# Kernel tuning notes

Hardware: AMD Instinct MI355X
Metric: run time of the kernel (lower is better)

The kernel has to match this reference:

```python
import jax, jax.numpy as jnp
import numpy as np

EPS = 1e-6

def _norm(x, alpha, beta):
    # torch std is unbiased (n-1); eps added to std (not var)
    d = x.shape[-1]
    mu = jnp.mean(x, axis=-1, keepdims=True)
    xc = x - mu
    std = jnp.sqrt(jnp.sum(xc * xc, axis=-1, keepdims=True) / (d - 1))
    return alpha * xc / (std + EPS) + beta

def setup_inputs() -> dict:
    key = jax.random.key(0)
    B, S, D, P, H, DFF = 4, 2048, 1024, 256, 16, 512
    ks = jax.random.split(key, 24)
    sd = 1.0 / np.sqrt(D)
    inp = {
        "feature_x": jax.random.normal(ks[0], (B, S, D), jnp.float32),
        "param_x": jax.random.normal(ks[1], (B, S, P), jnp.float32),
        "Wq": jax.random.normal(ks[2], (D, D), jnp.float32) * sd,
        "bq": jnp.zeros((D,), jnp.float32),
        "Wk": jax.random.normal(ks[3], (D, D), jnp.float32) * sd,
        "bk": jnp.zeros((D,), jnp.float32),
        "Wv": jax.random.normal(ks[4], (D, D), jnp.float32) * sd,
        "bv": jnp.zeros((D,), jnp.float32),
        "Wo": jax.random.normal(ks[5], (D, D), jnp.float32) * sd,
        "bo": jnp.zeros((D,), jnp.float32),
        "alpha1": jnp.ones((D,), jnp.float32),
        "beta1": jnp.zeros((D,), jnp.float32),
        "alpha2": jnp.ones((D,), jnp.float32),
        "beta2": jnp.zeros((D,), jnp.float32),
        "W1": jax.random.normal(ks[6], (D, DFF), jnp.float32) * sd,
        "b1": jnp.zeros((DFF,), jnp.float32),
        "W2": jax.random.normal(ks[7], (DFF, D), jnp.float32) / np.sqrt(DFF),
        "b2": jnp.zeros((D,), jnp.float32),
        "Wp": jax.random.normal(ks[8], (D + P, P), jnp.float32) / np.sqrt(D + P),
        "bp": jnp.zeros((P,), jnp.float32),
    }
    return inp

def reference(feature_x, param_x, Wq, bq, Wk, bk, Wv, bv, Wo, bo,
              alpha1, beta1, alpha2, beta2, W1, b1, W2, b2, Wp, bp):
    B, S, D = feature_x.shape
    H = 16
    dh = D // H
    # pre-norm (note: original reassigns feature_x = norm_1(feature_x))
    xn = _norm(feature_x, alpha1, beta1)
    q = (xn @ Wq + bq).reshape(B, S, H, dh)
    k = (xn @ Wk + bk).reshape(B, S, H, dh)
    v = (xn @ Wv + bv).reshape(B, S, H, dh)
    scores = jnp.einsum('bqhd,bkhd->bhqk', q, k) / jnp.sqrt(jnp.float32(dh))
    attn = jax.nn.softmax(scores, axis=-1)  # dropout = identity (eval)
    ctx = jnp.einsum('bhqk,bkhd->bqhd', attn, v).reshape(B, S, D)
    attn_out = ctx @ Wo + bo
    x = xn + attn_out
    x2 = _norm(x, alpha2, beta2)
    ff = jax.nn.relu(x2 @ W1 + b1) @ W2 + b2
    x = x + ff
    combined = jnp.concatenate([x, param_x], axis=-1)
    p = combined @ Wp + bp
    return (x, p)
```

## Files before the change

### kernel.cpp

```cpp
#include <hip/hip_runtime.h>
#include <hip/hip_bf16.h>

typedef unsigned short u16;
typedef short short8 __attribute__((ext_vector_type(8)));
typedef float f32x4 __attribute__((ext_vector_type(4)));

#define MELEM 8388608u
__device__ u16 g_ws[(size_t)MELEM * 13];

__device__ __forceinline__ float b2f(u16 u) {
  union { unsigned int i; float f; } v; v.i = ((unsigned int)u) << 16; return v.f;
}
__device__ __forceinline__ u16 f2b(float f) {
  union { float f; unsigned int i; } v; v.f = f;
  return (u16)((v.i + 0x7FFFu + ((v.i >> 16) & 1u)) >> 16);
}
__device__ __forceinline__ unsigned int pk2(float a, float b) {
  union { __hip_bfloat162 h; unsigned int u; } v;
  v.h = __float22bfloat162_rn(make_float2(a, b));
  return v.u;
}
__device__ __forceinline__ f32x4 mfma16(short8 a, short8 b, f32x4 c) {
  return __builtin_amdgcn_mfma_f32_16x16x32_bf16(a, b, c, 0, 0, 0);
}

typedef __attribute__((address_space(3))) unsigned int lds_u32;
typedef const __attribute__((address_space(1))) unsigned int glb_u32;
__device__ __forceinline__ void gld16(u16* l, const u16* g) {
  __builtin_amdgcn_global_load_lds((glb_u32*)g, (lds_u32*)l, 16, 0, 0);
}

#if __has_builtin(__builtin_amdgcn_exp2f)
#define QSCALE 0.18033688011112042f
#define SCLAMP 86.561714f
#define FEXP(x) __builtin_amdgcn_exp2f(x)
#else
#define QSCALE 0.125f
#define SCLAMP 60.0f
#define FEXP(x) __expf(x)
#endif

__device__ __forceinline__ void tr32(const float* __restrict__ W, u16* __restrict__ Wt,
                                     int K, int N, int bx, int by, int tid,
                                     float (*tile)[33]) {
  const int tx = tid & 31, ty = tid >> 5;
#pragma unroll
  for (int i = 0; i < 32; i += 8)
    tile[ty + i][tx] = W[(size_t)(by + ty + i) * N + bx + tx];
  __syncthreads();
#pragma unroll
  for (int i = 0; i < 32; i += 8)
    Wt[(size_t)(bx + ty + i) * K + by + tx] = f2b(tile[tx][ty + i]);
}

__global__ __launch_bounds__(256) void prep_kernel(
    const float* __restrict__ Wq, const float* __restrict__ Wk,
    const float* __restrict__ Wv, const float* __restrict__ Wo,
    const float* __restrict__ W1, const float* __restrict__ W2,
    const float* __restrict__ Wp,
    const float* __restrict__ bq, const float* __restrict__ bk,
    const float* __restrict__ bv, const float* __restrict__ param_x,
    u16* __restrict__ Wqkvt, u16* __restrict__ Wot, u16* __restrict__ W1t,
    u16* __restrict__ W2t, u16* __restrict__ Wpt,
    float* __restrict__ bqkv, u16* __restrict__ px_b) {
  __shared__ float tile[32][33];
  const int bid = blockIdx.x;
  const int tid = threadIdx.x;
  if (bid < 4096) {
    const int j = bid >> 10, r = bid & 1023;
    const int bx = (r & 31) * 32, by = (r >> 5) * 32;
    const float* src = (j == 0) ? Wq : (j == 1) ? Wk : (j == 2) ? Wv : Wo;
    u16* dst = (j == 3) ? Wot : (Wqkvt + (size_t)j * 1024 * 1024);
    tr32(src, dst, 1024, 1024, bx, by, tid, tile);
  } else if (bid < 4608) {
    const int r = bid - 4096;
    tr32(W1, W1t, 1024, 512, (r & 15) * 32, (r >> 4) * 32, tid, tile);
  } else if (bid < 5120) {
    const int r = bid - 4608;
    tr32(W2, W2t, 512, 1024, (r & 31) * 32, (r >> 5) * 32, tid, tile);
  } else if (bid < 5440) {
    const int r = bid - 5120;
    tr32(Wp, Wpt, 1280, 256, (r & 7) * 32, (r >> 3) * 32, tid, tile);
  } else if (bid < 5452) {
    const int i = (bid - 5440) * 256 + tid;
    bqkv[i] = (i < 1024) ? bq[i] : (i < 2048) ? bk[i - 1024] : bv[i - 2048];
  } else {
    const int i = (bid - 5452) * 256 + tid;
    px_b[i] = f2b(param_x[i]);
  }
}

__global__ __launch_bounds__(256) void ln_kernel(const float* __restrict__ x,
                                                 const float* __restrict__ alpha,
                                                 const float* __restrict__ beta,
                                                 u16* __restrict__ outb,
                                                 float* __restrict__ outf) {
  const int D = 1024;
  const int row = blockIdx.x;
  const int tid = threadIdx.x;
  const float4 u = *(const float4*)(x + (size_t)row * D + tid * 4);
  float s1 = u.x + u.y + u.z + u.w;
  float s2 = u.x * u.x + u.y * u.y + u.z * u.z + u.w * u.w;
#pragma unroll
  for (int off = 32; off >= 1; off >>= 1) {
    s1 += __shfl_xor(s1, off, 64);
    s2 += __shfl_xor(s2, off, 64);
  }
  __shared__ float ws1[4], ws2[4];
  if ((tid & 63) == 0) { ws1[tid >> 6] = s1; ws2[tid >> 6] = s2; }
  __syncthreads();
  s1 = ws1[0] + ws1[1] + ws1[2] + ws1[3];
  s2 = ws2[0] + ws2[1] + ws2[2] + ws2[3];
  const float mean = s1 * (1.0f / 1024.0f);
  const float var = fmaxf((s2 - 1024.0f * mean * mean) * (1.0f / 1023.0f), 0.0f);
  const float inv = 1.0f / (sqrtf(var) + 1e-6f);
  const float4 a = *(const float4*)(alpha + tid * 4);
  const float4 b = *(const float4*)(beta + tid * 4);
  const float o0 = a.x * (u.x - mean) * inv + b.x;
  const float o1 = a.y * (u.y - mean) * inv + b.y;
  const float o2 = a.z * (u.z - mean) * inv + b.z;
  const float o3 = a.w * (u.w - mean) * inv + b.w;
  ushort4 ob; ob.x = f2b(o0); ob.y = f2b(o1); ob.z = f2b(o2); ob.w = f2b(o3);
  *(ushort4*)(outb + (size_t)row * D + tid * 4) = ob;
  if (outf) {
    float4 of; of.x = o0; of.y = o1; of.z = o2; of.w = o3;
    *(float4*)(outf + (size_t)row * D + tid * 4) = of;
  }
}

template<int TM, int TN>
__global__ __launch_bounds__(256) void gemm_t(
    const u16* __restrict__ A, const u16* __restrict__ A2,
    const u16* __restrict__ Bt, const float* __restrict__ bias,
    const float* __restrict__ resid, float* __restrict__ Cf, u16* __restrict__ Cb,
    u16* __restrict__ Vt_out,
    int M, int N, int K, int K1, int relu, int ldcb) {
  __shared__ __align__(16) u16 As[TM * 32];
  __shared__ __align__(16) u16 Bs[TN * 32];
  const int tid = threadIdx.x;
  const int bn = blockIdx.x * TN;
  const int bm = blockIdx.y * TM;
  const int wv = tid >> 6, lane = tid & 63, quad = lane >> 4, l16 = lane & 15;
  constexpr int WN = (TM == 128) ? 64 : TN / 4;
  constexpr int AM = 4, AN = WN / 16;
  const int wm = (TM == 128) ? (wv >> 1) * 64 : 0;
  const int wn = (TM == 128) ? (wv & 1) * 64 : wv * WN;
  const int r0 = tid >> 2;
  const int cc = (tid & 3) * 8;
  f32x4 acc[AM][AN];
#pragma unroll
  for (int i = 0; i < AM; ++i)
#pragma unroll
    for (int j = 0; j < AN; ++j) acc[i][j] = (f32x4){0.f, 0.f, 0.f, 0.f};

  for (int k0 = 0; k0 < K; k0 += 32) {
    const u16* aS; int lda, kk;
    if (A2 != nullptr && k0 >= K1) { aS = A2; lda = K - K1; kk = k0 - K1; }
    else { aS = A; lda = (A2 != nullptr) ? K1 : K; kk = k0; }
#pragma unroll
    for (int i = 0; i < TM / 64; ++i)
      gld16(&As[i * 2048 + tid * 8], aS + (size_t)(bm + i * 64 + r0) * lda + kk + cc);
#pragma unroll
    for (int i = 0; i < TN / 64; ++i)
      gld16(&Bs[i * 2048 + tid * 8], Bt + (size_t)(bn + i * 64 + r0) * K + k0 + cc);
    __syncthreads();
    short8 af[AM], bf[AN];
#pragma unroll
    for (int mi = 0; mi < AM; ++mi)
      af[mi] = *(const short8*)&As[(wm + mi * 16 + l16) * 32 + quad * 8];
#pragma unroll
    for (int ni = 0; ni < AN; ++ni)
      bf[ni] = *(const short8*)&Bs[(wn + ni * 16 + l16) * 32 + quad * 8];
#pragma unroll
    for (int mi = 0; mi < AM; ++mi)
#pragma unroll
      for (int ni = 0; ni < AN; ++ni)
        acc[mi][ni] = mfma16(af[mi], bf[ni], acc[mi][ni]);
    __syncthreads();
  }

#pragma unroll
  for (int ni = 0; ni < AN; ++ni) {
    const int col = bn + wn + ni * 16 + l16;
    const float bb = bias ? bias[col] : 0.0f;
#pragma unroll
    for (int mi = 0; mi < AM; ++mi) {
      if (Vt_out != nullptr && col >= 2048) {
        const int s0 = bm + wm + mi * 16 + quad * 4;
        const int bb_idx = s0 >> 11;
        const size_t voff = ((size_t)(bb_idx * 1024 + col - 2048) << 11) + (s0 & 2047);
        ushort4 w;
        w.x = f2b(acc[mi][ni][0] + bb);
        w.y = f2b(acc[mi][ni][1] + bb);
        w.z = f2b(acc[mi][ni][2] + bb);
        w.w = f2b(acc[mi][ni][3] + bb);
        *(ushort4*)(Vt_out + voff) = w;
      } else {
#pragma unroll
        for (int r = 0; r < 4; ++r) {
          const int row = bm + wm + mi * 16 + quad * 4 + r;
          const size_t off = (size_t)row * N + col;
          float v = acc[mi][ni][r] + bb;
          if (resid) v += resid[off];
          if (relu) v = fmaxf(v, 0.0f);
          if (Cf) Cf[off] = v;
          if (Cb) Cb[(size_t)row * ldcb + col] = f2b(v);
        }
      }
    }
  }
}

__global__ __launch_bounds__(512) void attn_kernel(
    const u16* __restrict__ Q, const u16* __restrict__ Kb,
    const u16* __restrict__ Vtg, u16* __restrict__ O, int ldq) {
  const int S = 2048, NT = 32;
  __shared__ __align__(16) u16 Ks[2][64][64];
  __shared__ __align__(16) u16 Vs[2][64][64];
  __shared__ __align__(16) u16 Pb[8][32][40];
  const int tid = threadIdx.x;
  const int swz = ((blockIdx.x & 7) << 6) | (blockIdx.x >> 3);
  const int qt = swz & 7;
  const int bh = swz >> 3;
  const int b = bh >> 4, h = bh & 15;
  const int wv = tid >> 6, lane = tid & 63, quad = lane >> 4, l16 = lane & 15;
  const size_t brow = (size_t)b * S;
  const size_t hoff = (size_t)h * 64;
  const int q0 = qt * 256 + wv * 32;
  const u16* Vg = Vtg + (((size_t)(b * 1024 + h * 64)) << 11);

  short8 qf[2][2];
#pragma unroll
  for (int ni = 0; ni < 2; ++ni)
#pragma unroll
    for (int ks = 0; ks < 2; ++ks) {
      int4 t = *(const int4*)(Q + (brow + q0 + ni * 16 + l16) * ldq + hoff + ks * 32 + quad * 8);
      const u16* p = (const u16*)&t;
      short8 f;
#pragma unroll
      for (int j = 0; j < 8; ++j) f[j] = (short)f2b(b2f(p[j]) * QSCALE);
      qf[ni][ks] = f;
    }

  f32x4 oacc[4][2];
#pragma unroll
  for (int mi = 0; mi < 4; ++mi)
#pragma unroll
    for (int ni = 0; ni < 2; ++ni) oacc[mi][ni] = (f32x4){0.f, 0.f, 0.f, 0.f};
  float lsum[2] = {0.0f, 0.0f};
  const f32x4 z4 = {0.f, 0.f, 0.f, 0.f};

  const int srow = tid >> 3;
  const int sc = (tid & 7) ^ (srow & 7);

  gld16(&Ks[0][0][0] + (size_t)tid * 8, Kb + (brow + srow) * ldq + hoff + sc * 8);
  gld16(&Vs[0][0][0] + (size_t)tid * 8, Vg + ((size_t)srow << 11) + sc * 8);
  __syncthreads();

  for (int t = 0; t < NT; ++t) {
    const int p = t & 1, np = p ^ 1;
    if (t + 1 < NT) {
      const int kbn = (t + 1) * 64;
      gld16(&Ks[np][0][0] + (size_t)tid * 8, Kb + (brow + kbn + srow) * ldq + hoff + sc * 8);
      gld16(&Vs[np][0][0] + (size_t)tid * 8, Vg + ((size_t)srow << 11) + kbn + sc * 8);
    }

    const u16* ksb = &Ks[p][0][0];
    const u16* vsb = &Vs[p][0][0];
#pragma unroll
    for (int kk = 0; kk < 2; ++kk) {
#pragma unroll
      for (int half = 0; half < 2; ++half) {
        const int m = (kk * 2 + half) * 16 + l16;
        short8 af0 = *(const short8*)(ksb + m * 64 + ((quad ^ (m & 7)) * 8));
        short8 af1 = *(const short8*)(ksb + m * 64 + (((4 + quad) ^ (m & 7)) * 8));
#pragma unroll
        for (int ni = 0; ni < 2; ++ni) {
          f32x4 s = z4;
          s = mfma16(af0, qf[ni][0], s);
          s = mfma16(af1, qf[ni][1], s);
          const float e0 = FEXP(fminf(s[0], SCLAMP));
          const float e1 = FEXP(fminf(s[1], SCLAMP));
          const float e2 = FEXP(fminf(s[2], SCLAMP));
          const float e3 = FEXP(fminf(s[3], SCLAMP));
          lsum[ni] += (e0 + e1) + (e2 + e3);
          uint2 pk;
          pk.x = pk2(e0, e1);
          pk.y = pk2(e2, e3);
          *(uint2*)&Pb[wv][ni * 16 + l16][half * 16 + quad * 4] = pk;
        }
      }
      short8 pf[2];
#pragma unroll
      for (int ni = 0; ni < 2; ++ni)
        pf[ni] = *(const short8*)&Pb[wv][ni * 16 + l16][quad * 8];
      __builtin_amdgcn_s_setprio(1);
#pragma unroll
      for (int mi2 = 0; mi2 < 4; ++mi2) {
        const int dh = mi2 * 16 + l16;
        short8 vf = *(const short8*)(vsb + dh * 64 + (((kk * 4 + quad) ^ (dh & 7)) * 8));
#pragma unroll
        for (int ni = 0; ni < 2; ++ni)
          oacc[mi2][ni] = mfma16(vf, pf[ni], oacc[mi2][ni]);
      }
      __builtin_amdgcn_s_setprio(0);
    }

    if (t + 1 < NT) __syncthreads();
  }

#pragma unroll
  for (int ni = 0; ni < 2; ++ni) {
    lsum[ni] += __shfl_xor(lsum[ni], 16, 64);
    lsum[ni] += __shfl_xor(lsum[ni], 32, 64);
  }
#pragma unroll
  for (int ni = 0; ni < 2; ++ni) {
    const float rl = 1.0f / lsum[ni];
    const size_t ob = (brow + q0 + ni * 16 + l16) * 1024 + hoff;
#pragma unroll
    for (int mi2 = 0; mi2 < 4; ++mi2) {
      uint2 ov;
      ov.x = pk2(oacc[mi2][ni][0] * rl, oacc[mi2][ni][1] * rl);
      ov.y = pk2(oacc[mi2][ni][2] * rl, oacc[mi2][ni][3] * rl);
      *(uint2*)(O + ob + mi2 * 16 + quad * 4) = ov;
    }
  }
}

extern "C" void kernel_launch(void* const* d_in, const int* in_sizes, int n_in,
                              void* d_out, int out_size, void* d_ws, size_t ws_size,
                              hipStream_t stream) {
  const int M = 8192, D = 1024, P = 256, DFF = 512;

  const float* feature_x = (const float*)d_in[0];
  const float* param_x   = (const float*)d_in[1];
  const float* Wq = (const float*)d_in[2];  const float* bq = (const float*)d_in[3];
  const float* Wk = (const float*)d_in[4];  const float* bk = (const float*)d_in[5];
  const float* Wv = (const float*)d_in[6];  const float* bv = (const float*)d_in[7];
  const float* Wo = (const float*)d_in[8];  const float* bo = (const float*)d_in[9];
  const float* alpha1 = (const float*)d_in[10]; const float* beta1 = (const float*)d_in[11];
  const float* alpha2 = (const float*)d_in[12]; const float* beta2 = (const float*)d_in[13];
  const float* W1 = (const float*)d_in[14]; const float* b1 = (const float*)d_in[15];
  const float* W2 = (const float*)d_in[16]; const float* b2 = (const float*)d_in[17];
  const float* Wp = (const float*)d_in[18]; const float* bp = (const float*)d_in[19];

  void* sym = nullptr;
  hipGetSymbolAddress(&sym, HIP_SYMBOL(g_ws));
  u16* s = (u16*)sym;

  u16* xn_b   = s + (size_t)MELEM * 0;
  float* xn_f = (float*)(s + (size_t)MELEM * 1);
  u16* qkv_b  = s + (size_t)MELEM * 3;
  u16* vt     = s + (size_t)MELEM * 5;
  u16* ctx    = s + (size_t)MELEM * 6;
  float* x1_f = (float*)(s + (size_t)MELEM * 7);
  u16* x2_b   = s + (size_t)MELEM * 9;
  u16* h1_b   = s + (size_t)MELEM * 10;
  u16* xcp_b  = s + (size_t)MELEM * 11;
  u16* wreg   = s + (size_t)MELEM * 12;
  u16* px_b   = wreg;
  u16* Wqkvt  = px_b + 2097152;
  u16* Wot    = Wqkvt + 3145728;
  u16* W1t    = Wot + 1048576;
  u16* W2t    = W1t + 524288;
  u16* Wpt    = W2t + 524288;
  float* bqkv = (float*)(Wpt + 327680);

  float* xout_f = (float*)d_out;
  float* pout_f = xout_f + (size_t)M * D;

  dim3 blk(256);
  prep_kernel<<<13644, blk, 0, stream>>>(Wq, Wk, Wv, Wo, W1, W2, Wp, bq, bk, bv,
                                         param_x, Wqkvt, Wot, W1t, W2t, Wpt,
                                         bqkv, px_b);

  ln_kernel<<<M, blk, 0, stream>>>(feature_x, alpha1, beta1, xn_b, xn_f);
  gemm_t<128, 128><<<dim3(24, 64), blk, 0, stream>>>(xn_b, nullptr, Wqkvt, bqkv, nullptr,
                                                     nullptr, qkv_b, vt,
                                                     M, 3072, D, D, 0, 2048);
  attn_kernel<<<512, dim3(512), 0, stream>>>(qkv_b, qkv_b + 1024, vt, ctx, 2048);
  gemm_t<128, 128><<<dim3(8, 64), blk, 0, stream>>>(ctx, nullptr, Wot, bo, xn_f,
                                                    x1_f, nullptr, nullptr,
                                                    M, D, D, D, 0, D);
  ln_kernel<<<M, blk, 0, stream>>>(x1_f, alpha2, beta2, x2_b, nullptr);
  gemm_t<64, 128><<<dim3(4, 128), blk, 0, stream>>>(x2_b, nullptr, W1t, b1, nullptr,
                                                    nullptr, h1_b, nullptr,
                                                    M, DFF, D, D, 1, DFF);
  gemm_t<128, 128><<<dim3(8, 64), blk, 0, stream>>>(h1_b, nullptr, W2t, b2, x1_f,
                                                    xout_f, xcp_b, nullptr,
                                                    M, D, DFF, DFF, 0, D);
  gemm_t<64, 64><<<dim3(4, 128), blk, 0, stream>>>(xcp_b, px_b, Wpt, bp, nullptr,
                                                   pout_f, nullptr, nullptr,
                                                   M, P, D + P, D, 0, P);
}
```

Before: 539.0 us.

## Widen GEMM K-tile to 64, XOR-swizzle LDS, remap blocks across XCDs

Doubles the K step of the bf16 MFMA GEMM to 64, which halves the number of barrier pairs per output tile. LDS rows are stored with an XOR swizzle of the 16-byte column chunk to avoid bank conflicts on the fragment reads. It also remaps block IDs so that consecutive blocks on the same XCD cover neighbouring N tiles, to improve L2 reuse. In exchange the kernel uses twice the shared memory per block, which may lower occupancy, and it now assumes K is a multiple of 64.

```diff
diff --git a/kernel.cpp b/kernel.cpp
--- a/kernel.cpp
+++ b/kernel.cpp
@@ -135,47 +135,62 @@
     const float* __restrict__ resid, float* __restrict__ Cf, u16* __restrict__ Cb,
     u16* __restrict__ Vt_out,
     int M, int N, int K, int K1, int relu, int ldcb) {
-  __shared__ __align__(16) u16 As[TM * 32];
-  __shared__ __align__(16) u16 Bs[TN * 32];
+  __shared__ __align__(16) u16 As[TM * 64];
+  __shared__ __align__(16) u16 Bs[TN * 64];
   const int tid = threadIdx.x;
-  const int bn = blockIdx.x * TN;
-  const int bm = blockIdx.y * TM;
+  const int nx = gridDim.x;
+  int bxi, byi;
+  if ((nx & 7) == 0) {
+    const int bid = blockIdx.y * nx + blockIdx.x;
+    const int xcd = bid & 7, idx = bid >> 3, nxl = nx >> 3;
+    bxi = xcd * nxl + idx % nxl;
+    byi = idx / nxl;
+  } else { bxi = blockIdx.x; byi = blockIdx.y; }
+  const int bn = bxi * TN;
+  const int bm = byi * TM;
   const int wv = tid >> 6, lane = tid & 63, quad = lane >> 4, l16 = lane & 15;
+  const int lx = l16 & 7;
   constexpr int WN = (TM == 128) ? 64 : TN / 4;
   constexpr int AM = 4, AN = WN / 16;
   const int wm = (TM == 128) ? (wv >> 1) * 64 : 0;
   const int wn = (TM == 128) ? (wv & 1) * 64 : wv * WN;
-  const int r0 = tid >> 2;
-  const int cc = (tid & 3) * 8;
   f32x4 acc[AM][AN];
 #pragma unroll
   for (int i = 0; i < AM; ++i)
 #pragma unroll
     for (int j = 0; j < AN; ++j) acc[i][j] = (f32x4){0.f, 0.f, 0.f, 0.f};
 
-  for (int k0 = 0; k0 < K; k0 += 32) {
+  for (int k0 = 0; k0 < K; k0 += 64) {
     const u16* aS; int lda, kk;
     if (A2 != nullptr && k0 >= K1) { aS = A2; lda = K - K1; kk = k0 - K1; }
     else { aS = A; lda = (A2 != nullptr) ? K1 : K; kk = k0; }
 #pragma unroll
-    for (int i = 0; i < TM / 64; ++i)
-      gld16(&As[i * 2048 + tid * 8], aS + (size_t)(bm + i * 64 + r0) * lda + kk + cc);
-#pragma unroll
-    for (int i = 0; i < TN / 64; ++i)
-      gld16(&Bs[i * 2048 + tid * 8], Bt + (size_t)(bn + i * 64 + r0) * K + k0 + cc);
+    for (int i = 0; i < TM / 32; ++i) {
+      const int s = i * 256 + tid, row = s >> 3, cb = s & 7;
+      gld16(&As[s * 8], aS + (size_t)(bm + row) * lda + kk + ((cb ^ (row & 7)) * 8));
+    }
+#pragma unroll
+    for (int i = 0; i < TN / 32; ++i) {
+      const int s = i * 256 + tid, row = s >> 3, cb = s & 7;
+      gld16(&Bs[s * 8], Bt + (size_t)(bn + row) * K + k0 + ((cb ^ (row & 7)) * 8));
+    }
     __syncthreads();
-    short8 af[AM], bf[AN];
-#pragma unroll
-    for (int mi = 0; mi < AM; ++mi)
-      af[mi] = *(const short8*)&As[(wm + mi * 16 + l16) * 32 + quad * 8];
-#pragma unroll
-    for (int ni = 0; ni < AN; ++ni)
-      bf[ni] = *(const short8*)&Bs[(wn + ni * 16 + l16) * 32 + quad * 8];
-#pragma unroll
-    for (int mi = 0; mi < AM; ++mi)
+#pragma unroll
+    for (int kkh = 0; kkh < 2; ++kkh) {
+      const int jq = ((kkh << 2) | quad) ^ lx;
+      short8 af[AM], bf[AN];
+#pragma unroll
+      for (int mi = 0; mi < AM; ++mi)
+        af[mi] = *(const short8*)&As[(wm + mi * 16 + l16) * 64 + jq * 8];
 #pragma unroll
       for (int ni = 0; ni < AN; ++ni)
-        acc[mi][ni] = mfma16(af[mi], bf[ni], acc[mi][ni]);
+        bf[ni] = *(const short8*)&Bs[(wn + ni * 16 + l16) * 64 + jq * 8];
+#pragma unroll
+      for (int mi = 0; mi < AM; ++mi)
+#pragma unroll
+        for (int ni = 0; ni < AN; ++ni)
+          acc[mi][ni] = mfma16(af[mi], bf[ni], acc[mi][ni]);
+    }
     __syncthreads();
   }
 
```

Measured after the change: 454.1 us. 1.19x faster.
